# Optimization experiments

Hardware: AMD Instinct MI355X
Metric: run time of the kernel (lower is better)

## Reference

```python
import jax, jax.numpy as jnp
import numpy as np

B, CIN, L, D, H, DK, DV, K, KE = 8, 16, 256, 256, 8, 32, 32, 3, 5
EPS = 1e-9

def r2c(p):
    return p[..., 0] + 1j * p[..., 1]

def c2r(z):
    return jnp.stack([jnp.real(z), jnp.imag(z)], axis=-1)

def conv1d(x, w):
    # x: [B,C,L] complex, w: [O,C,Kt] complex, 'same' padding (pad = K//2)
    kt = w.shape[-1]; pad = kt // 2; Lx = x.shape[-1]
    xp = jnp.pad(x, ((0, 0), (0, 0), (pad, pad)))
    return sum(jnp.einsum('bcl,oc->bol', xp[:, :, i:i + Lx], w[:, :, i]) for i in range(kt))

def eca(x, w):
    # Efficient Channel Attention (complex): global avg pool over length,
    # 1D conv (kernel KE) across channels, split sigmoid gate, rescale.
    C = x.shape[1]; pad = w.shape[0] // 2
    y = x.mean(axis=-1)                              # [B,C] complex
    yp = jnp.pad(y, ((0, 0), (pad, pad)))
    z = sum(w[i] * yp[:, i:i + C] for i in range(w.shape[0]))
    a = jax.nn.sigmoid(z.real) + 1j * jax.nn.sigmoid(z.imag)
    return x * a[:, :, None]

def magminmax(s):
    # MagMinMaxNorm: min-max normalize magnitudes along last dim, keep phase.
    mag = jnp.abs(s)
    mn = mag.min(axis=-1, keepdims=True)
    mx = mag.max(axis=-1, keepdims=True)
    return s * (((mag - mn) / (mx - mn + EPS)) / (mag + EPS))

def mha(qi, ki, vi, Wq, Wk, Wv, Wo):
    # qi/ki/vi: [B, L, D] complex
    b, lq, _ = qi.shape
    q = jnp.einsum('bld,de->ble', qi, Wq).reshape(b, lq, H, DK)
    k = jnp.einsum('bld,de->ble', ki, Wk).reshape(b, -1, H, DK)
    v = jnp.einsum('bld,de->ble', vi, Wv).reshape(b, -1, H, DV)
    s = jnp.einsum('bqhd,bkhd->bhqk', q, k) * (1.0 / DK ** 0.5)
    o = jnp.einsum('bhqk,bkhd->bqhd', magminmax(s), v).reshape(b, lq, H * DV)
    return jnp.einsum('ble,ed->bld', o, Wo)

def ssca(A, Bx, Wq, Wk, Wv, Wo, eca_w, conv_w):
    # A, Bx: [B, D, L] complex. Wq/Wk/Wv/Wo indexed [AA, BB, AB, BA].
    At = jnp.swapaxes(A, 1, 2)
    Bt = jnp.swapaxes(Bx, 1, 2)
    Waa = mha(At, At, At, Wq[0], Wk[0], Wv[0], Wo[0])
    Xbb = mha(Bt, Bt, Bt, Wq[1], Wk[1], Wv[1], Wo[1])
    Yab = mha(At, Bt, Bt, Wq[2], Wk[2], Wv[2], Wo[2])
    Zba = mha(Bt, At, At, Wq[3], Wk[3], Wv[3], Wo[3])
    # cat along sequence dim (dim=1 pre-transpose in torch), then back to [B, D, 4L]
    Xc = jnp.swapaxes(jnp.concatenate([Waa, Xbb, Yab, Zba], axis=1), 1, 2)
    return conv1d(eca(Xc, eca_w), conv_w)

def fusion(X1, X2, head_w, head_b, wq, wk, wv, wo, ssca_eca_w, ssca_conv_w, top_eca_w):
    X1c, X2c = r2c(X1), r2c(X2)
    hw, hb = r2c(head_w), r2c(head_b)
    Wq, Wk, Wv, Wo = r2c(wq), r2c(wk), r2c(wv), r2c(wo)
    se, sc, te = r2c(ssca_eca_w), r2c(ssca_conv_w), r2c(top_eca_w)
    A = conv1d(X1c, hw[0]) + hb[0][None, :, None]
    Bc = conv1d(X2c, hw[1]) + hb[1][None, :, None]
    R = ssca(A, Bc, Wq[0], Wk[0], Wv[0], Wo[0], se[0], sc[0])
    kk = ssca(jnp.fft.ifft(A, axis=-1), jnp.fft.ifft(Bc, axis=-1),
              Wq[1], Wk[1], Wv[1], Wo[1], se[1], sc[1])
    R2 = jnp.concatenate([R, jnp.fft.fft(kk, axis=-1)], axis=1)      # [B, 2D, 4L]
    k2 = jnp.concatenate([kk, jnp.fft.ifft(R2[:, :D], axis=-1)], axis=1)
    return eca(R2, te[0]), eca(k2, te[1])

def setup_inputs() -> dict:
    key = jax.random.key(0)
    ks = jax.random.split(key, 11)
    def rn(k, shape, s=1.0):
        return jax.random.normal(k, shape, dtype=jnp.float32) * s
    wscale = 1.0 / D ** 0.5
    return {
        'X1': rn(ks[0], (B, CIN, L, 2)),
        'X2': rn(ks[1], (B, CIN, L, 2)),
        'head_w': rn(ks[2], (2, D, CIN, K, 2), 0.1),
        'head_b': rn(ks[3], (2, D, 2), 0.1),
        'wq': rn(ks[4], (2, 4, D, H * DK, 2), wscale),
        'wk': rn(ks[5], (2, 4, D, H * DK, 2), wscale),
        'wv': rn(ks[6], (2, 4, D, H * DV, 2), wscale),
        'wo': rn(ks[7], (2, 4, H * DV, D, 2), wscale),
        'ssca_eca_w': rn(ks[8], (2, KE, 2), 0.3),
        'ssca_conv_w': rn(ks[9], (2, D, D, K, 2), wscale),
        'top_eca_w': rn(ks[10], (2, KE, 2), 0.3),
    }

def reference(X1, X2, head_w, head_b, wq, wk, wv, wo, ssca_eca_w, ssca_conv_w, top_eca_w):
    Rc, kc = fusion(X1, X2, head_w, head_b, wq, wk, wv, wo, ssca_eca_w, ssca_conv_w, top_eca_w)
    return c2r(Rc), c2r(kc)
```

## Files before the change

### kernel.cpp

```cpp
#include <hip/hip_runtime.h>
#include <math.h>

namespace {

constexpr int Bn = 8, CINn = 16, Ln = 256, Dn = 256, Hn = 8, DKn = 32, DVn = 32;
constexpr int KWn = 3, KEn = 5, L4n = 1024;
constexpr float EPSf = 1e-9f;
constexpr int XP = 1040;
constexpr int LP = 40;

typedef __attribute__((ext_vector_type(8))) short short8b;
typedef __attribute__((ext_vector_type(4))) float f32x4;

__device__ __forceinline__ float2 cmul(float2 a, float2 b){
  return make_float2(a.x*b.x - a.y*b.y, a.x*b.y + a.y*b.x);
}
__device__ __forceinline__ float2 cfma(float2 a, float2 b, float2 c){
  c.x = fmaf(a.x, b.x, c.x); c.x = fmaf(-a.y, b.y, c.x);
  c.y = fmaf(a.x, b.y, c.y); c.y = fmaf(a.y, b.x, c.y);
  return c;
}
__device__ __forceinline__ ushort f2bf(float f){
  uint u = __float_as_uint(f);
  u += 0x7fffu + ((u >> 16) & 1u);
  return (ushort)(u >> 16);
}
__device__ __forceinline__ uint cvt_pk_bf16(float a, float b){
  uint u;
  asm("v_cvt_pk_bf16_f32 %0, %1, %2" : "=v"(u) : "v"(a), "v"(b));
  return u;
}
__device__ __forceinline__ short8b neg8(short8b v){
  union { short8b s; uint u[4]; } x; x.s = v;
  #pragma unroll
  for (int i = 0; i < 4; ++i) x.u[i] ^= 0x80008000u;
  return x.s;
}

__global__ void head_conv_kernel(const float2* __restrict__ X, const float2* __restrict__ hw,
                                 const float2* __restrict__ hb, float2* __restrict__ out){
  int idx = blockIdx.x * blockDim.x + threadIdx.x;
  if (idx >= Bn*Dn*Ln) return;
  int l = idx & (Ln-1);
  int o = (idx >> 8) & (Dn-1);
  int b = idx >> 16;
  float2 acc = hb[o];
  for (int c = 0; c < CINn; ++c){
    const float2* xr = X + (size_t)(b*CINn + c)*Ln;
    const float2* wr = hw + (size_t)(o*CINn + c)*KWn;
    #pragma unroll
    for (int i = 0; i < KWn; ++i){
      int ll = l + i - 1;
      if (ll >= 0 && ll < Ln) acc = cfma(xr[ll], wr[i], acc);
    }
  }
  out[idx] = acc;
}

template<int N, int LOG>
__global__ void fft_rows_kernel(const float2* __restrict__ src0, float2* __restrict__ dst0,
                                int schans, int scoff, int dchans, int dcoff,
                                float sign, float scale, float2* __restrict__ ysum){
  __shared__ float2 buf[N];
  __shared__ float2 tw[N/2];
  __shared__ float rx[256], ry[256];
  int row = blockIdx.x;
  int rb = row >> 8, rc = row & 255;
  const float2* src = src0 + (size_t)(rb*schans + scoff + rc)*N;
  float2* dst = dst0 + (size_t)(rb*dchans + dcoff + rc)*N;
  int tid = threadIdx.x;
  for (int i = tid; i < N/2; i += 256){
    float a = sign * 6.2831853071795864f * (float)i / (float)N;
    float s, c; __sincosf(a, &s, &c);
    tw[i] = make_float2(c, s);
  }
  for (int i = tid; i < N; i += 256){
    unsigned r = __brev((unsigned)i) >> (32 - LOG);
    buf[r] = src[i];
  }
  __syncthreads();
  for (int st = 1; st <= LOG; ++st){
    int half = 1 << (st-1);
    for (int bf = tid; bf < N/2; bf += 256){
      int blk = bf >> (st-1);
      int pos = bf & (half-1);
      int i0 = (blk << st) + pos;
      int i1 = i0 + half;
      float2 w = tw[pos << (LOG-st)];
      float2 u = buf[i0];
      float2 t = cmul(w, buf[i1]);
      buf[i0] = make_float2(u.x + t.x, u.y + t.y);
      buf[i1] = make_float2(u.x - t.x, u.y - t.y);
    }
    __syncthreads();
  }
  float sx = 0.f, sy = 0.f;
  for (int i = tid; i < N; i += 256){
    float2 o = make_float2(buf[i].x * scale, buf[i].y * scale);
    dst[i] = o; sx += o.x; sy += o.y;
  }
  if (ysum){
    rx[tid] = sx; ry[tid] = sy; __syncthreads();
    for (int st = 128; st > 0; st >>= 1){
      if (tid < st){ rx[tid] += rx[tid+st]; ry[tid] += ry[tid+st]; }
      __syncthreads();
    }
    if (tid == 0)
      ysum[(size_t)rb*dchans + dcoff + rc] = make_float2(rx[0]*(1.f/N), ry[0]*(1.f/N));
  }
}

__global__ void row_mean_map(const float2* __restrict__ src0, int schans, int scoff,
                             float2* __restrict__ y, int dchans, int dcoff){
  int row = blockIdx.x;
  int rb = row >> 8, rc = row & 255;
  const float2* xr = src0 + (size_t)(rb*schans + scoff + rc)*L4n;
  int tid = threadIdx.x;
  float sx = 0.f, sy = 0.f;
  for (int i = tid; i < L4n; i += 256){ float2 v = xr[i]; sx += v.x; sy += v.y; }
  __shared__ float rx[256], ry[256];
  rx[tid] = sx; ry[tid] = sy; __syncthreads();
  for (int st = 128; st > 0; st >>= 1){
    if (tid < st){ rx[tid] += rx[tid+st]; ry[tid] += ry[tid+st]; }
    __syncthreads();
  }
  if (tid == 0)
    y[(size_t)rb*dchans + dcoff + rc] = make_float2(rx[0]*(1.f/L4n), ry[0]*(1.f/L4n));
}

__device__ __forceinline__ void cgemm_core(
    const ushort* __restrict__ Are, const ushort* __restrict__ Aim, int pitchA, int am0,
    const ushort* __restrict__ Bre, const ushort* __restrict__ Bim, int pitchB, int n0,
    int K, int conv, float2* __restrict__ cbase, size_t crow, int cmode,
    ushort* __restrict__ ore, ushort* __restrict__ oim)
{
  __shared__ ushort sh[16896];
  ushort* As_re = sh;
  ushort* As_im = sh + 5120;
  ushort* Bs_re = sh + 10240;
  ushort* Bs_im = sh + 12800;
  int tid = threadIdx.x;
  int lane = tid & 63, w = tid >> 6;
  int lrow = lane & 15, lhalf = lane >> 4;
  f32x4 ar[2][4], ai[2][4];
  #pragma unroll
  for (int s = 0; s < 2; ++s)
    #pragma unroll
    for (int t = 0; t < 4; ++t){ ar[s][t] = (f32x4){0,0,0,0}; ai[s][t] = (f32x4){0,0,0,0}; }
  int nk = K >> 5;
  for (int kc = 0; kc < nk; ++kc){
    int k0 = kc << 5;
    __syncthreads();
    #pragma unroll
    for (int rep = 0; rep < 4; ++rep){
      int q = tid + rep*256;
      int row = q >> 3, kq = (q & 7)*4;
      size_t go = (size_t)(am0 + row)*pitchA + k0 + kq;
      *(uint2*)&As_re[row*LP + kq] = *(const uint2*)&Are[go];
      *(uint2*)&As_im[row*LP + kq] = *(const uint2*)&Aim[go];
    }
    if (!conv){
      #pragma unroll
      for (int rep = 0; rep < 2; ++rep){
        int q = tid + rep*256;
        int row = q >> 3, kq = (q & 7)*4;
        size_t go = (size_t)(n0 + row)*pitchB + k0 + kq;
        *(uint2*)&Bs_re[row*LP + kq] = *(const uint2*)&Bre[go];
        *(uint2*)&Bs_im[row*LP + kq] = *(const uint2*)&Bim[go];
      }
    } else {
      #pragma unroll
      for (int rep = 0; rep < 8; ++rep){
        int idx = tid + rep*256;
        int k = idx >> 6, nn = idx & 63;
        uint kk = (uint)(k0 + k);
        uint c = (kk * 0xAAABu) >> 17;
        int i = (int)(kk - c*3u);
        size_t go = (size_t)c*XP + 8 + n0 + nn + i - 1;
        Bs_re[nn*LP + k] = Bre[go];
        Bs_im[nn*LP + k] = Bim[go];
      }
    }
    __syncthreads();
    short8b afr[2], afi[2], bfr[4], bfi[4];
    #pragma unroll
    for (int s = 0; s < 2; ++s){
      int row = w*32 + s*16 + lrow;
      afr[s] = *(const short8b*)&As_re[row*LP + lhalf*8];
      afi[s] = *(const short8b*)&As_im[row*LP + lhalf*8];
    }
    #pragma unroll
    for (int t = 0; t < 4; ++t){
      int row = t*16 + lrow;
      bfr[t] = *(const short8b*)&Bs_re[row*LP + lhalf*8];
      bfi[t] = *(const short8b*)&Bs_im[row*LP + lhalf*8];
    }
    #pragma unroll
    for (int s = 0; s < 2; ++s){
      short8b ain = neg8(afi[s]);
      #pragma unroll
      for (int t = 0; t < 4; ++t){
        ar[s][t] = __builtin_amdgcn_mfma_f32_16x16x32_bf16(ain,    bfi[t], ar[s][t], 0, 0, 0);
        ar[s][t] = __builtin_amdgcn_mfma_f32_16x16x32_bf16(afr[s], bfr[t], ar[s][t], 0, 0, 0);
        ai[s][t] = __builtin_amdgcn_mfma_f32_16x16x32_bf16(afi[s], bfr[t], ai[s][t], 0, 0, 0);
        ai[s][t] = __builtin_amdgcn_mfma_f32_16x16x32_bf16(afr[s], bfi[t], ai[s][t], 0, 0, 0);
      }
    }
  }
  if (cmode == 0){
    #pragma unroll
    for (int s = 0; s < 2; ++s)
      #pragma unroll
      for (int t = 0; t < 4; ++t)
        #pragma unroll
        for (int r = 0; r < 4; ++r){
          int mm = w*32 + s*16 + lhalf*4 + r;
          int nn = t*16 + lrow;
          if (ore){
            ore[(size_t)mm*crow + nn] = f2bf(ar[s][t][r]);
            oim[(size_t)mm*crow + nn] = f2bf(ai[s][t][r]);
          } else {
            cbase[(size_t)mm*crow + nn] = make_float2(ar[s][t][r], ai[s][t][r]);
          }
        }
  } else if (cmode == 2 || cmode == 3){
    #pragma unroll
    for (int s = 0; s < 2; ++s)
      #pragma unroll
      for (int t = 0; t < 4; ++t)
        #pragma unroll
        for (int r = 0; r < 4; ++r){
          int mm = w*32 + s*16 + lhalf*4 + r;
          int nn = t*16 + lrow;
          int gl = am0 + mm, ge = n0 + nn;
          size_t oidx;
          if (cmode == 2)
            oidx = (((size_t)(ge >> 5))*Ln + gl)*32 + (ge & 31);
          else
            oidx = (((size_t)(ge >> 5))*8 + (gl >> 5))*1024 + (size_t)(ge & 31)*32 + (gl & 31);
          ore[oidx] = f2bf(ar[s][t][r]);
          oim[oidx] = f2bf(ai[s][t][r]);
        }
  } else {
    float2* T = (float2*)sh;
    #pragma unroll
    for (int h2 = 0; h2 < 2; ++h2){
      __syncthreads();
      #pragma unroll
      for (int s = 0; s < 2; ++s)
        #pragma unroll
        for (int t2 = 0; t2 < 2; ++t2){
          int t = h2*2 + t2;
          #pragma unroll
          for (int r = 0; r < 4; ++r){
            int mm = w*32 + s*16 + lhalf*4 + r;
            int nn = t2*16 + lrow;
            T[mm*33 + nn] = make_float2(ar[s][t][r], ai[s][t][r]);
          }
        }
      __syncthreads();
      #pragma unroll
      for (int rep = 0; rep < 16; ++rep){
        int idx = tid + rep*256;
        int mm = idx & 127, nn = idx >> 7;
        float2 v = T[mm*33 + nn];
        if (ore){
          ore[(size_t)(h2*32 + nn)*crow + mm] = f2bf(v.x);
          oim[(size_t)(h2*32 + nn)*crow + mm] = f2bf(v.y);
        } else {
          cbase[(size_t)(h2*32 + nn)*crow + mm] = v;
        }
      }
    }
  }
}

__global__ __launch_bounds__(256) void qkv_mfma(
    const ushort* __restrict__ aAre, const ushort* __restrict__ aAim,
    const ushort* __restrict__ aBre, const ushort* __restrict__ aBim,
    const ushort* __restrict__ WqRe, const ushort* __restrict__ WqIm,
    const ushort* __restrict__ WkRe, const ushort* __restrict__ WkIm,
    const ushort* __restrict__ WvRe, const ushort* __restrict__ WvIm,
    ushort* __restrict__ QpRe, ushort* __restrict__ QpIm,
    ushort* __restrict__ KpRe, ushort* __restrict__ KpIm,
    ushort* __restrict__ VpRe, ushort* __restrict__ VpIm,
    int set, int m0, size_t pstride)
{
  int my = blockIdx.y;
  int ml = my / 3, which = my - ml*3;
  int m = m0 + ml;
  bool useA = (which == 0) ? (m == 0 || m == 2) : (m == 0 || m == 3);
  const ushort* Are = useA ? aAre : aBre;
  const ushort* Aim = useA ? aAim : aBim;
  const ushort* WRe = (which == 0) ? WqRe : (which == 1) ? WkRe : WvRe;
  const ushort* WIm = (which == 0) ? WqIm : (which == 1) ? WkIm : WvIm;
  size_t woff = (size_t)(set*4 + m)*Dn*Dn;
  int bx = blockIdx.x;
  int nt = bx & 3, mt = (bx >> 2) & 1, b = bx >> 3;
  int l0 = mt*128, e0 = nt*64;
  const ushort* ARe = Are + (size_t)b*Ln*Dn;
  const ushort* AIm = Aim + (size_t)b*Ln*Dn;
  size_t po = (size_t)ml*pstride + (size_t)b*Ln*Dn;
  if (which == 2){
    cgemm_core(ARe, AIm, Dn, l0, WRe + woff, WIm + woff, Dn, e0, Dn, 0,
               nullptr, 0, 3, VpRe + po, VpIm + po);
  } else {
    ushort* orp = ((which == 0) ? QpRe : KpRe) + po;
    ushort* oip = ((which == 0) ? QpIm : KpIm) + po;
    cgemm_core(ARe, AIm, Dn, l0, WRe + woff, WIm + woff, Dn, e0, Dn, 0,
               nullptr, 0, 2, orp, oip);
  }
}

__global__ __launch_bounds__(256) void wo_mfma(
    const ushort* __restrict__ ORe, const ushort* __restrict__ OIm,
    const ushort* __restrict__ WoRe, const ushort* __restrict__ WoIm,
    float2* __restrict__ Xc, int set, int m0)
{
  int ml = blockIdx.y;
  int m = m0 + ml;
  size_t woff = (size_t)(set*4 + m)*Dn*Dn;
  int bx = blockIdx.x;
  int nt = bx & 3, mt = (bx >> 2) & 1, b = bx >> 3;
  int l0 = mt*128, d0 = nt*64;
  const ushort* ARe = ORe + ((size_t)ml*Bn + b)*Ln*Dn;
  const ushort* AIm = OIm + ((size_t)ml*Bn + b)*Ln*Dn;
  float2* cb = Xc + ((size_t)b*Dn + d0)*L4n + m*Ln + l0;
  cgemm_core(ARe, AIm, Dn, l0, WoRe + woff, WoIm + woff, Dn, d0, Dn, 0,
             cb, L4n, 1, nullptr, nullptr);
}

__global__ __launch_bounds__(256) void conv_mfma(
    const ushort* __restrict__ WRe, const ushort* __restrict__ WIm,
    const ushort* __restrict__ XRe, const ushort* __restrict__ XIm,
    float2* __restrict__ out, int ochans)
{
  int bx = blockIdx.x;
  int xt = bx & 15, ot = (bx >> 4) & 1, b = bx >> 5;
  int o0 = ot*128, x0 = xt*64;
  const ushort* xr = XRe + (size_t)b*Dn*XP;
  const ushort* xi = XIm + (size_t)b*Dn*XP;
  float2* cb = out + ((size_t)(b*ochans) + o0)*L4n + x0;
  cgemm_core(WRe, WIm, 768, o0, xr, xi, XP, x0, 768, 1, cb, L4n, 0,
             nullptr, nullptr);
}

__global__ __launch_bounds__(256) void attn_mfma(
    const ushort* __restrict__ QRe, const ushort* __restrict__ QIm,
    const ushort* __restrict__ KRe, const ushort* __restrict__ KIm,
    const ushort* __restrict__ VRe, const ushort* __restrict__ VIm,
    ushort* __restrict__ ORe, ushort* __restrict__ OIm, size_t pstride)
{
  size_t po = (size_t)blockIdx.y*pstride;
  const ushort* qre = QRe + po; const ushort* qim = QIm + po;
  const ushort* kre = KRe + po; const ushort* kim = KIm + po;
  const ushort* vre = VRe + po; const ushort* vim = VIm + po;
  ushort* ore = ORe + po; ushort* oim = OIm + po;
  int bx = blockIdx.x;
  int qt = bx >> 6, h = (bx >> 3) & 7, b = bx & 7;
  int q0 = qt*16;
  int tid = threadIdx.x;
  int lane = tid & 63, w = tid >> 6;
  int lg = lane >> 4, lr = lane & 15;
  __shared__ float4 shm4[1056];
  __shared__ float2 mmb[4][4][4];
  ushort* PsRe = (ushort*)shm4;
  ushort* PsIm = PsRe + 4224;
  float2* redbuf = (float2*)shm4;
  const float scl = 0.17677669529663687f;
  size_t hbase = (size_t)(b*Hn + h)*Ln*32;

  size_t qoff = hbase + (size_t)(q0 + lr)*32 + lg*8;
  short8b aqr = *(const short8b*)&qre[qoff];
  short8b aqi = *(const short8b*)&qim[qoff];
  short8b aqin = neg8(aqi);

  f32x4 sr[4], si[4];
  #pragma unroll
  for (int t = 0; t < 4; ++t){ sr[t] = (f32x4){0,0,0,0}; si[t] = (f32x4){0,0,0,0}; }
  #pragma unroll
  for (int t = 0; t < 4; ++t){
    int kcol = w*64 + t*16 + lr;
    size_t koff = hbase + (size_t)kcol*32 + lg*8;
    short8b bkr = *(const short8b*)&kre[koff];
    short8b bki = *(const short8b*)&kim[koff];
    sr[t] = __builtin_amdgcn_mfma_f32_16x16x32_bf16(aqin, bki, sr[t], 0, 0, 0);
    sr[t] = __builtin_amdgcn_mfma_f32_16x16x32_bf16(aqr,  bkr, sr[t], 0, 0, 0);
    si[t] = __builtin_amdgcn_mfma_f32_16x16x32_bf16(aqi,  bkr, si[t], 0, 0, 0);
    si[t] = __builtin_amdgcn_mfma_f32_16x16x32_bf16(aqr,  bki, si[t], 0, 0, 0);
  }
  float s2a[4][4];
  float mn2[4], mx2[4];
  #pragma unroll
  for (int r = 0; r < 4; ++r){ mn2[r] = 3.4e38f; mx2[r] = 0.f; }
  #pragma unroll
  for (int t = 0; t < 4; ++t)
    #pragma unroll
    for (int r = 0; r < 4; ++r){
      float x = sr[t][r]*scl, y = si[t][r]*scl;
      sr[t][r] = x; si[t][r] = y;
      float s2 = fmaf(x, x, y*y);
      s2a[t][r] = s2;
      mn2[r] = fminf(mn2[r], s2); mx2[r] = fmaxf(mx2[r], s2);
    }
  #pragma unroll
  for (int off = 1; off < 16; off <<= 1)
    #pragma unroll
    for (int r = 0; r < 4; ++r){
      mn2[r] = fminf(mn2[r], __shfl_xor(mn2[r], off));
      mx2[r] = fmaxf(mx2[r], __shfl_xor(mx2[r], off));
    }
  if (lr == 0){
    #pragma unroll
    for (int r = 0; r < 4; ++r) mmb[w][lg][r] = make_float2(mn2[r], mx2[r]);
  }
  __syncthreads();
  float mnv[4], invr[4];
  #pragma unroll
  for (int r = 0; r < 4; ++r){
    float2 v0 = mmb[0][lg][r], v1 = mmb[1][lg][r];
    float2 v2 = mmb[2][lg][r], v3 = mmb[3][lg][r];
    float fmn2 = fminf(fminf(v0.x, v1.x), fminf(v2.x, v3.x));
    float fmx2 = fmaxf(fmaxf(v0.y, v1.y), fmaxf(v2.y, v3.y));
    mnv[r] = sqrtf(fmn2);
    invr[r] = __builtin_amdgcn_rcpf(sqrtf(fmx2) - mnv[r] + EPSf);
  }
  #pragma unroll
  for (int t = 0; t < 4; ++t)
    #pragma unroll
    for (int r = 0; r < 4; ++r){
      int q = lg*4 + r, k = w*64 + t*16 + lr;
      float m = sqrtf(s2a[t][r]);
      float f = (m - mnv[r])*invr[r]*__builtin_amdgcn_rcpf(m + EPSf);
      uint u = cvt_pk_bf16(sr[t][r]*f, si[t][r]*f);
      PsRe[q*264 + k] = (ushort)u;
      PsIm[q*264 + k] = (ushort)(u >> 16);
    }
  f32x4 pr[2], pi[2];
  #pragma unroll
  for (int t = 0; t < 2; ++t){ pr[t] = (f32x4){0,0,0,0}; pi[t] = (f32x4){0,0,0,0}; }
  #pragma unroll
  for (int kc = 0; kc < 2; ++kc){
    int k0 = w*64 + kc*32;
    short8b par = *(const short8b*)&PsRe[lr*264 + k0 + lg*8];
    short8b pai = *(const short8b*)&PsIm[lr*264 + k0 + lg*8];
    short8b pain = neg8(pai);
    #pragma unroll
    for (int t = 0; t < 2; ++t){
      int dv = t*16 + lr;
      size_t voff = hbase + (size_t)(k0 >> 5)*1024 + dv*32 + lg*8;
      short8b bvr = *(const short8b*)&vre[voff];
      short8b bvi = *(const short8b*)&vim[voff];
      pr[t] = __builtin_amdgcn_mfma_f32_16x16x32_bf16(pain, bvi, pr[t], 0, 0, 0);
      pr[t] = __builtin_amdgcn_mfma_f32_16x16x32_bf16(par,  bvr, pr[t], 0, 0, 0);
      pi[t] = __builtin_amdgcn_mfma_f32_16x16x32_bf16(pai,  bvr, pi[t], 0, 0, 0);
      pi[t] = __builtin_amdgcn_mfma_f32_16x16x32_bf16(par,  bvi, pi[t], 0, 0, 0);
    }
  }
  __syncthreads();
  #pragma unroll
  for (int t = 0; t < 2; ++t)
    #pragma unroll
    for (int r = 0; r < 4; ++r)
      redbuf[(w*16 + lg*4 + r)*32 + t*16 + lr] = make_float2(pr[t][r], pi[t][r]);
  __syncthreads();
  #pragma unroll
  for (int rep = 0; rep < 2; ++rep){
    int idx = tid + rep*256;
    int q = idx >> 5, dv = idx & 31;
    float2 s0 = redbuf[(0*16 + q)*32 + dv], s1 = redbuf[(1*16 + q)*32 + dv];
    float2 s2 = redbuf[(2*16 + q)*32 + dv], s3 = redbuf[(3*16 + q)*32 + dv];
    float sx = s0.x + s1.x + s2.x + s3.x;
    float sy = s0.y + s1.y + s2.y + s3.y;
    size_t oo = ((size_t)(b*Ln + q0 + q))*Dn + h*DVn + dv;
    uint u = cvt_pk_bf16(sx, sy);
    ore[oo] = (ushort)u; oim[oo] = (ushort)(u >> 16);
  }
}

__global__ void pack_at(const float2* __restrict__ in, ushort* __restrict__ ore,
                        ushort* __restrict__ oim){
  __shared__ float2 T[32][33];
  int bx = blockIdx.x;
  int lt = bx & 7, dt = (bx >> 3) & 7, b = bx >> 6;
  int tid = threadIdx.x;
  int c = tid & 31, rr = tid >> 5;
  #pragma unroll
  for (int it = 0; it < 4; ++it){
    int d = rr + it*8;
    T[d][c] = in[((size_t)b*Dn + dt*32 + d)*Ln + lt*32 + c];
  }
  __syncthreads();
  #pragma unroll
  for (int it = 0; it < 4; ++it){
    int l = rr + it*8;
    float2 v = T[c][l];
    size_t o = ((size_t)b*Ln + lt*32 + l)*Dn + dt*32 + c;
    ore[o] = f2bf(v.x); oim[o] = f2bf(v.y);
  }
}

__global__ void pack_wt(const float2* __restrict__ wq, const float2* __restrict__ wk,
                        const float2* __restrict__ wv, const float2* __restrict__ wo,
                        ushort* r0, ushort* i0, ushort* r1, ushort* i1,
                        ushort* r2, ushort* i2, ushort* r3, ushort* i3){
  int f = blockIdx.y;
  const float2* in = (f == 0) ? wq : (f == 1) ? wk : (f == 2) ? wv : wo;
  ushort* orr = (f == 0) ? r0 : (f == 1) ? r1 : (f == 2) ? r2 : r3;
  ushort* oii = (f == 0) ? i0 : (f == 1) ? i1 : (f == 2) ? i2 : i3;
  int bx = blockIdx.x;
  int tile = bx & 63, mat = bx >> 6;
  int kt = tile & 7, nt = tile >> 3;
  __shared__ float2 T[32][33];
  int tid = threadIdx.x;
  int c = tid & 31, rr = tid >> 5;
  #pragma unroll
  for (int it = 0; it < 4; ++it){
    int k = rr + it*8;
    T[k][c] = in[((size_t)(mat*256 + kt*32 + k))*256 + nt*32 + c];
  }
  __syncthreads();
  #pragma unroll
  for (int it = 0; it < 4; ++it){
    int n = rr + it*8;
    float2 v = T[c][n];
    size_t o = ((size_t)(mat*256 + nt*32 + n))*256 + kt*32 + c;
    orr[o] = f2bf(v.x); oii[o] = f2bf(v.y);
  }
}

__global__ void pack_sc(const float2* __restrict__ sc, ushort* __restrict__ ore,
                        ushort* __restrict__ oim){
  size_t idx = (size_t)blockIdx.x*256 + threadIdx.x;
  float2 v = sc[idx];
  ore[idx] = f2bf(v.x); oim[idx] = f2bf(v.y);
}

__global__ void eca_apply_pack(const float2* __restrict__ X, const float2* __restrict__ g,
                               ushort* __restrict__ xre, ushort* __restrict__ xim){
  int idx = blockIdx.x*256 + threadIdx.x;
  int row = idx >> 10, x = idx & 1023;
  float2 v = cmul(X[idx], g[row]);
  size_t o = (size_t)row*XP + 8 + x;
  xre[o] = f2bf(v.x); xim[o] = f2bf(v.y);
  if (x < 8){ size_t o2 = (size_t)row*XP + x; xre[o2] = 0; xim[o2] = 0; }
  if (x >= 1016){ size_t o2 = (size_t)row*XP + x + 16; xre[o2] = 0; xim[o2] = 0; }
}

__global__ void eca_gate_kernel(const float2* __restrict__ y, const float2* __restrict__ w,
                                float2* __restrict__ g, int C){
  int idx = blockIdx.x*blockDim.x + threadIdx.x;
  if (idx >= Bn*C) return;
  int c = idx % C;
  int b = idx / C;
  float2 z = make_float2(0.f, 0.f);
  #pragma unroll
  for (int i = 0; i < KEn; ++i){
    int cc = c + i - 2;
    if (cc >= 0 && cc < C) z = cfma(w[i], y[b*C + cc], z);
  }
  g[idx] = make_float2(1.f/(1.f + expf(-z.x)), 1.f/(1.f + expf(-z.y)));
}

__global__ void eca_apply4(float4* __restrict__ X, const float2* __restrict__ g){
  int idx = blockIdx.x*256 + threadIdx.x;
  int row = idx >> 9;
  float2 gg = g[row];
  float4 v = X[idx];
  float2 a = cmul(make_float2(v.x, v.y), gg);
  float2 b = cmul(make_float2(v.z, v.w), gg);
  X[idx] = make_float4(a.x, a.y, b.x, b.y);
}

}

extern "C" void kernel_launch(void* const* d_in, const int* in_sizes, int n_in,
                              void* d_out, int out_size, void* d_ws, size_t ws_size,
                              hipStream_t stream){
  const float2* X1 = (const float2*)d_in[0];
  const float2* X2 = (const float2*)d_in[1];
  const float2* head_w = (const float2*)d_in[2];
  const float2* head_b = (const float2*)d_in[3];
  const float2* wq = (const float2*)d_in[4];
  const float2* wk = (const float2*)d_in[5];
  const float2* wv = (const float2*)d_in[6];
  const float2* wo = (const float2*)d_in[7];
  const float2* se = (const float2*)d_in[8];
  const float2* sc = (const float2*)d_in[9];
  const float2* te = (const float2*)d_in[10];

  const size_t SZ_BDL = (size_t)Bn*Dn*Ln;
  const size_t SZ_X   = (size_t)Bn*Dn*L4n;
  const size_t NAt    = (size_t)Bn*Ln*Dn;

  const size_t US_FIX = 2*(4*NAt) + 2*(4*8*(size_t)65536)
                      + 2*(2*(size_t)Dn*768) + 2*((size_t)Bn*Dn*XP);
  auto need_bytes = [&](int mc){
    return (SZ_X + 32768)*sizeof(float2)
         + (US_FIX + (size_t)8*mc*NAt)*sizeof(ushort);
  };
  int mcount = 2;
  if (ws_size >= need_bytes(4)) mcount = 4;

  float2* p = (float2*)d_ws;
  float2* Xc = p;  p += SZ_X;
  float2* ybufX = p; p += (size_t)Bn*Dn;
  float2* ybufR = p; p += (size_t)Bn*2*Dn;
  float2* ybufK = p; p += (size_t)Bn*2*Dn;
  float2* gbuf  = p; p += (size_t)Bn*2*Dn;

  ushort* us = (ushort*)p;
  auto grab = [&](size_t n){ ushort* r = us; us += n; return r; };
  ushort *AtRe[4], *AtIm[4];
  for (int i = 0; i < 4; ++i){ AtRe[i] = grab(NAt); AtIm[i] = grab(NAt); }
  ushort *WRe4[4], *WIm4[4];
  for (int f = 0; f < 4; ++f){ WRe4[f] = grab(8*(size_t)65536); WIm4[f] = grab(8*(size_t)65536); }
  ushort* ScRe = grab(2*(size_t)Dn*768);
  ushort* ScIm = grab(2*(size_t)Dn*768);
  ushort* XRe = grab((size_t)Bn*Dn*XP);
  ushort* XIm = grab((size_t)Bn*Dn*XP);
  ushort* QpRe = grab((size_t)mcount*NAt);
  ushort* QpIm = grab((size_t)mcount*NAt);
  ushort* KpRe = grab((size_t)mcount*NAt);
  ushort* KpIm = grab((size_t)mcount*NAt);
  ushort* VpRe = grab((size_t)mcount*NAt);
  ushort* VpIm = grab((size_t)mcount*NAt);
  ushort* ObRe = grab((size_t)mcount*NAt);
  ushort* ObIm = grab((size_t)mcount*NAt);

  float2* A  = (float2*)QpRe;
  float2* Bc = A  + SZ_BDL;
  float2* iA = Bc + SZ_BDL;
  float2* iB = iA + SZ_BDL;

  float2* out0 = (float2*)d_out;
  float2* out1 = out0 + (size_t)Bn*2*Dn*L4n;

  head_conv_kernel<<<(Bn*Dn*Ln)/256, 256, 0, stream>>>(X1, head_w, head_b, A);
  head_conv_kernel<<<(Bn*Dn*Ln)/256, 256, 0, stream>>>(
      X2, head_w + (size_t)Dn*CINn*KWn, head_b + Dn, Bc);

  fft_rows_kernel<256,8><<<Bn*Dn, 256, 0, stream>>>(A,  iA, 256,0,256,0, 1.0f, 1.0f/256.0f, nullptr);
  fft_rows_kernel<256,8><<<Bn*Dn, 256, 0, stream>>>(Bc, iB, 256,0,256,0, 1.0f, 1.0f/256.0f, nullptr);

  pack_at<<<512, 256, 0, stream>>>(A,  AtRe[0], AtIm[0]);
  pack_at<<<512, 256, 0, stream>>>(Bc, AtRe[1], AtIm[1]);
  pack_at<<<512, 256, 0, stream>>>(iA, AtRe[2], AtIm[2]);
  pack_at<<<512, 256, 0, stream>>>(iB, AtRe[3], AtIm[3]);
  pack_wt<<<dim3(512, 4), 256, 0, stream>>>(wq, wk, wv, wo,
      WRe4[0], WIm4[0], WRe4[1], WIm4[1], WRe4[2], WIm4[2], WRe4[3], WIm4[3]);
  pack_sc<<<1536, 256, 0, stream>>>(sc, ScRe, ScIm);

  auto run_ssca = [&](int ia, int ib, int set, float2* dstbase, float2* ybufT){
    for (int m0 = 0; m0 < 4; m0 += mcount){
      qkv_mfma<<<dim3(64, 3*mcount), 256, 0, stream>>>(
          AtRe[ia], AtIm[ia], AtRe[ib], AtIm[ib],
          WRe4[0], WIm4[0], WRe4[1], WIm4[1], WRe4[2], WIm4[2],
          QpRe, QpIm, KpRe, KpIm, VpRe, VpIm, set, m0, NAt);
      attn_mfma<<<dim3(Bn*Hn*16, mcount), 256, 0, stream>>>(
          QpRe, QpIm, KpRe, KpIm, VpRe, VpIm, ObRe, ObIm, NAt);
      wo_mfma<<<dim3(64, mcount), 256, 0, stream>>>(
          ObRe, ObIm, WRe4[3], WIm4[3], Xc, set, m0);
    }
    row_mean_map<<<Bn*Dn, 256, 0, stream>>>(Xc, Dn, 0, ybufX, Dn, 0);
    eca_gate_kernel<<<(Bn*Dn + 255)/256, 256, 0, stream>>>(ybufX, se + set*KEn, gbuf, Dn);
    eca_apply_pack<<<(int)(SZ_X/256), 256, 0, stream>>>(Xc, gbuf, XRe, XIm);
    conv_mfma<<<256, 256, 0, stream>>>(
        ScRe + (size_t)set*Dn*768, ScIm + (size_t)set*Dn*768, XRe, XIm, dstbase, 2*Dn);
    row_mean_map<<<Bn*Dn, 256, 0, stream>>>(dstbase, 2*Dn, 0, ybufT, 2*Dn, 0);
  };

  run_ssca(0, 1, 0, out0, ybufR);
  run_ssca(2, 3, 1, out1, ybufK);

  fft_rows_kernel<1024,10><<<Bn*Dn, 256, 0, stream>>>(out1, out0, 2*Dn,0, 2*Dn,Dn, -1.0f, 1.0f, ybufR);
  fft_rows_kernel<1024,10><<<Bn*Dn, 256, 0, stream>>>(out0, out1, 2*Dn,0, 2*Dn,Dn, 1.0f, 1.0f/1024.0f, ybufK);

  eca_gate_kernel<<<(Bn*2*Dn + 255)/256, 256, 0, stream>>>(ybufR, te, gbuf, 2*Dn);
  eca_apply4<<<(int)((size_t)Bn*2*Dn*L4n/2/256), 256, 0, stream>>>((float4*)out0, gbuf);
  eca_gate_kernel<<<(Bn*2*Dn + 255)/256, 256, 0, stream>>>(ybufK, te + KEn, gbuf, 2*Dn);
  eca_apply4<<<(int)((size_t)Bn*2*Dn*L4n/2/256), 256, 0, stream>>>((float4*)out1, gbuf);
}
```

Measured before the change: 392.7 us.

## Add 64x64 complex MFMA GEMM tile for Wo and conv kernels

New measurement: 484.0 us. 23.2% more time.

```diff
diff --git a/kernel.cpp b/kernel.cpp
--- a/kernel.cpp
+++ b/kernel.cpp
@@ -7,7 +7,7 @@
 constexpr int KWn = 3, KEn = 5, L4n = 1024;
 constexpr float EPSf = 1e-9f;
 constexpr int XP = 1040;
-constexpr int LP = 40;
+constexpr int LP = 44;
 
 typedef __attribute__((ext_vector_type(8))) short short8b;
 typedef __attribute__((ext_vector_type(4))) float f32x4;
@@ -136,9 +136,9 @@
 {
   __shared__ ushort sh[16896];
   ushort* As_re = sh;
-  ushort* As_im = sh + 5120;
-  ushort* Bs_re = sh + 10240;
-  ushort* Bs_im = sh + 12800;
+  ushort* As_im = sh + 128*LP;
+  ushort* Bs_re = sh + 256*LP;
+  ushort* Bs_im = sh + 320*LP;
   int tid = threadIdx.x;
   int lane = tid & 63, w = tid >> 6;
   int lrow = lane & 15, lhalf = lane >> 4;
@@ -223,7 +223,7 @@
             cbase[(size_t)mm*crow + nn] = make_float2(ar[s][t][r], ai[s][t][r]);
           }
         }
-  } else if (cmode == 2 || cmode == 3){
+  } else {
     #pragma unroll
     for (int s = 0; s < 2; ++s)
       #pragma unroll
@@ -241,35 +241,122 @@
           ore[oidx] = f2bf(ar[s][t][r]);
           oim[oidx] = f2bf(ai[s][t][r]);
         }
+  }
+}
+
+__device__ __forceinline__ void cgemm64_core(
+    const ushort* __restrict__ Are, const ushort* __restrict__ Aim, int pitchA, int am0,
+    const ushort* __restrict__ Bre, const ushort* __restrict__ Bim, int pitchB, int n0,
+    int K, int conv, float2* __restrict__ cbase, size_t crow, int cmode)
+{
+  __shared__ ushort sh[11264];
+  ushort* As_re = sh;
+  ushort* As_im = sh + 64*LP;
+  ushort* Bs_re = sh + 128*LP;
+  ushort* Bs_im = sh + 192*LP;
+  int tid = threadIdx.x;
+  int lane = tid & 63, w = tid >> 6;
+  int wm = w >> 1, wn = w & 1;
+  int lrow = lane & 15, lhalf = lane >> 4;
+  f32x4 ar[2][2], ai[2][2];
+  #pragma unroll
+  for (int s = 0; s < 2; ++s)
+    #pragma unroll
+    for (int t = 0; t < 2; ++t){ ar[s][t] = (f32x4){0,0,0,0}; ai[s][t] = (f32x4){0,0,0,0}; }
+  int nk = K >> 5;
+  for (int kc = 0; kc < nk; ++kc){
+    int k0 = kc << 5;
+    __syncthreads();
+    #pragma unroll
+    for (int rep = 0; rep < 2; ++rep){
+      int q = tid + rep*256;
+      int row = q >> 3, kq = (q & 7)*4;
+      size_t go = (size_t)(am0 + row)*pitchA + k0 + kq;
+      *(uint2*)&As_re[row*LP + kq] = *(const uint2*)&Are[go];
+      *(uint2*)&As_im[row*LP + kq] = *(const uint2*)&Aim[go];
+    }
+    if (!conv){
+      #pragma unroll
+      for (int rep = 0; rep < 2; ++rep){
+        int q = tid + rep*256;
+        int row = q >> 3, kq = (q & 7)*4;
+        size_t go = (size_t)(n0 + row)*pitchB + k0 + kq;
+        *(uint2*)&Bs_re[row*LP + kq] = *(const uint2*)&Bre[go];
+        *(uint2*)&Bs_im[row*LP + kq] = *(const uint2*)&Bim[go];
+      }
+    } else {
+      #pragma unroll
+      for (int rep = 0; rep < 8; ++rep){
+        int idx = tid + rep*256;
+        int k = idx >> 6, nn = idx & 63;
+        uint kk = (uint)(k0 + k);
+        uint c = (kk * 0xAAABu) >> 17;
+        int i = (int)(kk - c*3u);
+        size_t go = (size_t)c*XP + 8 + n0 + nn + i - 1;
+        Bs_re[nn*LP + k] = Bre[go];
+        Bs_im[nn*LP + k] = Bim[go];
+      }
+    }
+    __syncthreads();
+    short8b afr[2], afi[2], bfr[2], bfi[2];
+    #pragma unroll
+    for (int s = 0; s < 2; ++s){
+      int row = wm*32 + s*16 + lrow;
+      afr[s] = *(const short8b*)&As_re[row*LP + lhalf*8];
+      afi[s] = *(const short8b*)&As_im[row*LP + lhalf*8];
+    }
+    #pragma unroll
+    for (int t = 0; t < 2; ++t){
+      int row = wn*32 + t*16 + lrow;
+      bfr[t] = *(const short8b*)&Bs_re[row*LP + lhalf*8];
+      bfi[t] = *(const short8b*)&Bs_im[row*LP + lhalf*8];
+    }
+    #pragma unroll
+    for (int s = 0; s < 2; ++s){
+      short8b ain = neg8(afi[s]);
+      #pragma unroll
+      for (int t = 0; t < 2; ++t){
+        ar[s][t] = __builtin_amdgcn_mfma_f32_16x16x32_bf16(ain,    bfi[t], ar[s][t], 0, 0, 0);
+        ar[s][t] = __builtin_amdgcn_mfma_f32_16x16x32_bf16(afr[s], bfr[t], ar[s][t], 0, 0, 0);
+        ai[s][t] = __builtin_amdgcn_mfma_f32_16x16x32_bf16(afi[s], bfr[t], ai[s][t], 0, 0, 0);
+        ai[s][t] = __builtin_amdgcn_mfma_f32_16x16x32_bf16(afr[s], bfi[t], ai[s][t], 0, 0, 0);
+      }
+    }
+  }
+  if (cmode == 0){
+    #pragma unroll
+    for (int s = 0; s < 2; ++s)
+      #pragma unroll
+      for (int t = 0; t < 2; ++t)
+        #pragma unroll
+        for (int r = 0; r < 4; ++r){
+          int mm = wm*32 + s*16 + lhalf*4 + r;
+          int nn = wn*32 + t*16 + lrow;
+          cbase[(size_t)mm*crow + nn] = make_float2(ar[s][t][r], ai[s][t][r]);
+        }
   } else {
     float2* T = (float2*)sh;
     #pragma unroll
     for (int h2 = 0; h2 < 2; ++h2){
       __syncthreads();
-      #pragma unroll
-      for (int s = 0; s < 2; ++s)
+      if (wn == h2){
         #pragma unroll
-        for (int t2 = 0; t2 < 2; ++t2){
-          int t = h2*2 + t2;
+        for (int s = 0; s < 2; ++s)
           #pragma unroll
-          for (int r = 0; r < 4; ++r){
-            int mm = w*32 + s*16 + lhalf*4 + r;
-            int nn = t2*16 + lrow;
-            T[mm*33 + nn] = make_float2(ar[s][t][r], ai[s][t][r]);
-          }
-        }
+          for (int t = 0; t < 2; ++t)
+            #pragma unroll
+            for (int r = 0; r < 4; ++r){
+              int mm = wm*32 + s*16 + lhalf*4 + r;
+              int nn = t*16 + lrow;
+              T[mm*33 + nn] = make_float2(ar[s][t][r], ai[s][t][r]);
+            }
+      }
       __syncthreads();
       #pragma unroll
-      for (int rep = 0; rep < 16; ++rep){
+      for (int rep = 0; rep < 8; ++rep){
         int idx = tid + rep*256;
-        int mm = idx & 127, nn = idx >> 7;
-        float2 v = T[mm*33 + nn];
-        if (ore){
-          ore[(size_t)(h2*32 + nn)*crow + mm] = f2bf(v.x);
-          oim[(size_t)(h2*32 + nn)*crow + mm] = f2bf(v.y);
-        } else {
-          cbase[(size_t)(h2*32 + nn)*crow + mm] = v;
-        }
+        int mm = idx & 63, nn = idx >> 6;
+        cbase[(size_t)(h2*32 + nn)*crow + mm] = T[mm*33 + nn];
       }
     }
   }
@@ -321,13 +408,13 @@
   int m = m0 + ml;
   size_t woff = (size_t)(set*4 + m)*Dn*Dn;
   int bx = blockIdx.x;
-  int nt = bx & 3, mt = (bx >> 2) & 1, b = bx >> 3;
-  int l0 = mt*128, d0 = nt*64;
+  int nt = bx & 3, lt = (bx >> 2) & 3, b = bx >> 4;
+  int l0 = lt*64, d0 = nt*64;
   const ushort* ARe = ORe + ((size_t)ml*Bn + b)*Ln*Dn;
   const ushort* AIm = OIm + ((size_t)ml*Bn + b)*Ln*Dn;
   float2* cb = Xc + ((size_t)b*Dn + d0)*L4n + m*Ln + l0;
-  cgemm_core(ARe, AIm, Dn, l0, WoRe + woff, WoIm + woff, Dn, d0, Dn, 0,
-             cb, L4n, 1, nullptr, nullptr);
+  cgemm64_core(ARe, AIm, Dn, l0, WoRe + woff, WoIm + woff, Dn, d0, Dn, 0,
+               cb, L4n, 1);
 }
 
 __global__ __launch_bounds__(256) void conv_mfma(
@@ -336,13 +423,12 @@
     float2* __restrict__ out, int ochans)
 {
   int bx = blockIdx.x;
-  int xt = bx & 15, ot = (bx >> 4) & 1, b = bx >> 5;
-  int o0 = ot*128, x0 = xt*64;
+  int xt = bx & 15, ot = (bx >> 4) & 3, b = bx >> 6;
+  int o0 = ot*64, x0 = xt*64;
   const ushort* xr = XRe + (size_t)b*Dn*XP;
   const ushort* xi = XIm + (size_t)b*Dn*XP;
   float2* cb = out + ((size_t)(b*ochans) + o0)*L4n + x0;
-  cgemm_core(WRe, WIm, 768, o0, xr, xi, XP, x0, 768, 1, cb, L4n, 0,
-             nullptr, nullptr);
+  cgemm64_core(WRe, WIm, 768, o0, xr, xi, XP, x0, 768, 1, cb, L4n, 0);
 }
 
 __global__ __launch_bounds__(256) void attn_mfma(
@@ -659,13 +745,13 @@
           QpRe, QpIm, KpRe, KpIm, VpRe, VpIm, set, m0, NAt);
       attn_mfma<<<dim3(Bn*Hn*16, mcount), 256, 0, stream>>>(
           QpRe, QpIm, KpRe, KpIm, VpRe, VpIm, ObRe, ObIm, NAt);
-      wo_mfma<<<dim3(64, mcount), 256, 0, stream>>>(
+      wo_mfma<<<dim3(128, mcount), 256, 0, stream>>>(
           ObRe, ObIm, WRe4[3], WIm4[3], Xc, set, m0);
     }
     row_mean_map<<<Bn*Dn, 256, 0, stream>>>(Xc, Dn, 0, ybufX, Dn, 0);
     eca_gate_kernel<<<(Bn*Dn + 255)/256, 256, 0, stream>>>(ybufX, se + set*KEn, gbuf, Dn);
     eca_apply_pack<<<(int)(SZ_X/256), 256, 0, stream>>>(Xc, gbuf, XRe, XIm);
-    conv_mfma<<<256, 256, 0, stream>>>(
+    conv_mfma<<<512, 256, 0, stream>>>(
         ScRe + (size_t)set*Dn*768, ScIm + (size_t)set*Dn*768, XRe, XIm, dstbase, 2*Dn);
     row_mean_map<<<Bn*Dn, 256, 0, stream>>>(dstbase, 2*Dn, 0, ybufT, 2*Dn, 0);
   };
```
